# Kernel optimization log

Measured on AMD Instinct MI355X. Metric: run time of the kernel, lower is better.

The kernel has to match this reference:

```python
import jax, jax.numpy as jnp
import numpy as np

C = 5.0          # tanh clamp constant (args.c, non-trainable)
B, N, R, D = 4, 16, 64, 256  # batch, block_num, block_len, word_dim
NEG = -1e9


def setup_inputs() -> dict:
    key = jax.random.key(0)
    ks = iter(jax.random.split(key, 80))

    def W(i, o):
        # xavier-like init (torch stores (out,in); we store (in,out) and use x @ W)
        return jax.random.normal(next(ks), (i, o), jnp.float32) * np.float32(np.sqrt(2.0 / (i + o)))

    def bvec(d):
        return jax.random.normal(next(ks), (d,), jnp.float32) * 0.01

    inp = {"x": jax.random.normal(next(ks), (B, N, R, D), jnp.float32)}
    for p in ("fw", "bw"):
        inp[f"fcW_{p}"] = W(D, D);  inp[f"fcb_{p}"] = bvec(D)
        inp[f"mW1_{p}"] = W(D, D);  inp[f"mW2_{p}"] = W(D, D);  inp[f"mb_{p}"] = bvec(D)
        inp[f"s2tW1_{p}"] = W(D, D); inp[f"s2tb1_{p}"] = bvec(D)
        inp[f"s2tW_{p}"] = W(D, D);  inp[f"s2tb_{p}"] = bvec(D)
        inp[f"gW1_{p}"] = W(D, D);  inp[f"gW2_{p}"] = W(D, D);  inp[f"gb_{p}"] = bvec(D)
        inp[f"fW1_{p}"] = W(3 * D, D); inp[f"fb1_{p}"] = bvec(D)
        inp[f"fW2_{p}"] = W(3 * D, D); inp[f"fb2_{p}"] = bvec(D)
    return inp


def _mSA(x, W1, W2, b, fw):
    # x: (..., L, d) -> (..., L, d). Additive per-feature attention with strict
    # triangular mask. fw: token i attends to j > i (last row zeroed);
    # bw: token i attends to j < i (first row zeroed). Matches the torch
    # -inf mask + narrow + zero-pad construction exactly.
    L = x.shape[-2]
    xi = (x @ W1)[..., :, None, :]                 # (..., L, 1, d)
    xj = (x @ W2)[..., None, :, :]                 # (..., 1, L, d)
    f = C * jnp.tanh((xi + xj + b) / C)            # (..., i, j, d)
    i = jnp.arange(L)[:, None]
    j = jnp.arange(L)[None, :]
    allowed = (j > i) if fw else (j < i)           # (L, L)
    scores = jnp.where(allowed[..., None], f, NEG)
    att = jax.nn.softmax(scores, axis=-2)          # softmax over j
    rowvalid = (jnp.arange(L) < L - 1) if fw else (jnp.arange(L) > 0)
    att = att * rowvalid[:, None, None].astype(x.dtype)
    return jnp.einsum('...ijd,...jd->...id', att, x)


def _s2t(x, W1, b1, Wo, bo):
    # source2token self-attention: (..., L, d) -> (..., d)
    f = jax.nn.relu(x @ W1 + b1)
    a = jax.nn.softmax(f @ Wo + bo, axis=-2)
    return jnp.sum(a * x, axis=-2)


def _mblosa(x, mW1, mW2, mb, s2tW1, s2tb1, s2tW, s2tb,
            gW1, gW2, gb, fW1, fb1, fW2, fb2, fw):
    Bb, n, r, d = x.shape
    h = _mSA(x, mW1, mW2, mb, fw)                  # (B, n, r, d) intra-block
    v = _s2t(h, s2tW1, s2tb1, s2tW, s2tb)          # (B, n, d)    block summary
    o = _mSA(v, mW1, mW2, mb, fw)                  # (B, n, d)    inter-block
    G = jax.nn.sigmoid(o @ gW1 + v @ gW2 + gb)
    e = G * o + (1.0 - G) * v                      # (B, n, d)
    # torch: cat of e[i] repeated r times, then narrow(1, 0, n)
    idx = jnp.arange(n) // r
    E = e[:, idx]                                  # (B, n, d)
    # torch: flatten blocks then narrow(1, 0, n) (faithful to source)
    xf = x.reshape(Bb, n * r, d)[:, :n]
    hf = h.reshape(Bb, n * r, d)[:, :n]
    cat = jnp.concatenate([xf, hf, E], axis=-1)    # (B, n, 3d)
    fusion = jax.nn.relu(cat @ fW1 + fb1)
    Gf = jax.nn.sigmoid(cat @ fW2 + fb2)
    return Gf * fusion + (1.0 - Gf) * xf           # (B, n, d)


def reference(x,
              fcW_fw, fcb_fw, mW1_fw, mW2_fw, mb_fw, s2tW1_fw, s2tb1_fw,
              s2tW_fw, s2tb_fw, gW1_fw, gW2_fw, gb_fw, fW1_fw, fb1_fw,
              fW2_fw, fb2_fw,
              fcW_bw, fcb_bw, mW1_bw, mW2_bw, mb_bw, s2tW1_bw, s2tb1_bw,
              s2tW_bw, s2tb_bw, gW1_bw, gW2_bw, gb_bw, fW1_bw, fb1_bw,
              fW2_bw, fb2_bw):
    in_fw = jax.nn.relu(x @ fcW_fw + fcb_fw)
    in_bw = jax.nn.relu(x @ fcW_bw + fcb_bw)
    u_fw = _mblosa(in_fw, mW1_fw, mW2_fw, mb_fw, s2tW1_fw, s2tb1_fw,
                   s2tW_fw, s2tb_fw, gW1_fw, gW2_fw, gb_fw,
                   fW1_fw, fb1_fw, fW2_fw, fb2_fw, True)
    u_bw = _mblosa(in_bw, mW1_bw, mW2_bw, mb_bw, s2tW1_bw, s2tb1_bw,
                   s2tW_bw, s2tb_bw, gW1_bw, gW2_bw, gb_bw,
                   fW1_bw, fb1_bw, fW2_bw, fb2_bw, False)
    return jnp.concatenate([u_fw, u_bw], axis=-1)  # (B, n, 2d)
```

## Files before the change

kernel.cpp:

```cpp
#include <hip/hip_runtime.h>
#include <hip/hip_bf16.h>

typedef __hip_bfloat16 BF16;
typedef __attribute__((ext_vector_type(8))) short short8;
typedef __attribute__((ext_vector_type(4))) short short4v;
typedef __attribute__((ext_vector_type(4))) float f32x4;
typedef __attribute__((ext_vector_type(2))) float f32x2;

#define MFMA_B16(a,b,c) __builtin_amdgcn_mfma_f32_16x16x32_bf16((a),(b),(c),0,0,0)

#if __has_builtin(__builtin_amdgcn_exp2f)
#define EXP2F(x) __builtin_amdgcn_exp2f(x)
#else
#define EXP2F(x) __expf(0.6931471805599453f * (x))
#endif

__device__ __forceinline__ short f2bs(float f){ BF16 h = __float2bfloat16(f); return *(short*)&h; }
__device__ __forceinline__ float bs2f(short s){ BF16 h = *(BF16*)&s; return __bfloat162float(h); }

struct SrcPack { const float* s[10]; };

__global__ __launch_bounds__(256) void prep_k(SrcPack p, const float* __restrict__ xsrc,
    short* __restrict__ Oh, short* __restrict__ Ol,
    short* __restrict__ xH, short* __restrict__ xL)
{
    if (blockIdx.y < 10) {
        __shared__ float s[64][65];
        const float* W = p.s[blockIdx.y];
        short* oh = Oh + (size_t)blockIdx.y * 65536;
        short* ol = Ol + (size_t)blockIdx.y * 65536;
        int tr = (blockIdx.x >> 2) * 64, tc = (blockIdx.x & 3) * 64;
        #pragma unroll
        for (int i = 0; i < 16; i++) {
            int e = threadIdx.x + i * 256;
            int r = e >> 6, c = e & 63;
            s[c][r] = W[(size_t)(tr + r) * 256 + tc + c];
        }
        __syncthreads();
        #pragma unroll
        for (int i = 0; i < 16; i++) {
            int e = threadIdx.x + i * 256;
            int c2 = e >> 6, r2 = e & 63;
            float v = s[c2][r2];
            short hi = f2bs(v);
            short lo = f2bs(v - bs2f(hi));
            size_t oi = (size_t)(tc + c2) * 256 + tr + r2;
            oh[oi] = hi;
            ol[oi] = lo;
        }
    } else {
        size_t base0 = (size_t)(blockIdx.y - 10) * 524288
                     + (size_t)blockIdx.x * 32768 + threadIdx.x * 4;
        for (int it = 0; it < 32; it++) {
            size_t idx = base0 + (size_t)it * 1024;
            float4 f = *(const float4*)&xsrc[idx];
            float v[4] = {f.x, f.y, f.z, f.w};
            short4v h, lo;
            #pragma unroll
            for (int t = 0; t < 4; t++) {
                h[t] = f2bs(v[t]);
                lo[t] = f2bs(v[t] - bs2f(h[t]));
            }
            *(short4v*)&xH[idx] = h;
            *(short4v*)&xL[idx] = lo;
        }
    }
}

template<int AM, int OM, int RELU, int BS>
__device__ __forceinline__ void gemm_body(const void* __restrict__ A0,
    const void* __restrict__ Alo,
    const short* __restrict__ Wh, const short* __restrict__ Wl,
    const float* __restrict__ bias, void* __restrict__ O0, void* __restrict__ O1,
    int row0, int col0)
{
    constexpr int LDK = 72;
    __shared__ short sAh[64 * LDK];
    __shared__ short sAl[(AM == 0) ? 8 : 64 * LDK];
    __shared__ short sBh[64 * LDK];
    __shared__ short sBl[BS ? 8 : 64 * LDK];
    int tid = threadIdx.x;
    int w = tid >> 6, l = tid & 63;
    int m = l & 15, q = l >> 4;
    int sr = w * 16 + m;

    f32x4 acc[4];
    #pragma unroll
    for (int cf = 0; cf < 4; cf++) acc[cf] = (f32x4)(0.f);

    for (int kh = 0; kh < 4; kh++) {
        int kbase = kh * 64;
        #pragma unroll
        for (int i = 0; i < 2; i++) {
            int kl = q * 8 + 32 * i;
            size_t gofs = (size_t)(row0 + sr) * 256 + kbase + kl;
            if (AM == 1) {
                const float* src = (const float*)A0 + gofs;
                float4 f0 = *(const float4*)src;
                float4 f1 = *(const float4*)(src + 4);
                short8 vh, vl;
                float tmp[8] = {f0.x, f0.y, f0.z, f0.w, f1.x, f1.y, f1.z, f1.w};
                #pragma unroll
                for (int j = 0; j < 8; j++) {
                    vh[j] = f2bs(tmp[j]);
                    vl[j] = f2bs(tmp[j] - bs2f(vh[j]));
                }
                *(short8*)&sAh[sr * LDK + kl] = vh;
                *(short8*)&sAl[sr * LDK + kl] = vl;
            } else if (AM == 2) {
                *(short8*)&sAh[sr * LDK + kl] = *(const short8*)((const short*)A0 + gofs);
                *(short8*)&sAl[sr * LDK + kl] = *(const short8*)((const short*)Alo + gofs);
            } else {
                *(short8*)&sAh[sr * LDK + kl] = *(const short8*)((const short*)A0 + gofs);
            }
            size_t gofsB = (size_t)(col0 + sr) * 256 + kbase + kl;
            *(short8*)&sBh[sr * LDK + kl] = *(const short8*)(Wh + gofsB);
            if (!BS)
                *(short8*)&sBl[sr * LDK + kl] = *(const short8*)(Wl + gofsB);
        }
        __syncthreads();
        #pragma unroll
        for (int ch = 0; ch < 2; ch++) {
            int k = ch * 32 + q * 8;
            short8 ah = *(const short8*)&sAh[(w * 16 + m) * LDK + k];
            short8 al = (AM != 0) ? *(const short8*)&sAl[(w * 16 + m) * LDK + k] : ah;
            #pragma unroll
            for (int cf = 0; cf < 4; cf++) {
                short8 bh = *(const short8*)&sBh[(cf * 16 + m) * LDK + k];
                acc[cf] = MFMA_B16(ah, bh, acc[cf]);
                if (!BS) {
                    short8 bl = *(const short8*)&sBl[(cf * 16 + m) * LDK + k];
                    acc[cf] = MFMA_B16(ah, bl, acc[cf]);
                }
                if (AM != 0)
                    acc[cf] = MFMA_B16(al, bh, acc[cf]);
            }
        }
        __syncthreads();
    }
    #pragma unroll
    for (int cf = 0; cf < 4; cf++) {
        int col = col0 + cf * 16 + m;
        float bv = bias ? bias[col] : 0.f;
        #pragma unroll
        for (int r = 0; r < 4; r++) {
            int row = row0 + w * 16 + q * 4 + r;
            float v = acc[cf][r] + bv;
            if (RELU) v = fmaxf(v, 0.f);
            size_t oi = (size_t)row * 256 + col;
            if (OM == 0) {
                ((float*)O0)[oi] = v;
            } else if (OM == 1) {
                ((short*)O0)[oi] = f2bs(v);
            } else {
                short hi = f2bs(v);
                ((short*)O0)[oi] = hi;
                ((short*)O1)[oi] = f2bs(v - bs2f(hi));
            }
        }
    }
}

struct GDir { const void* A0; const void* Al; const short* Wh; const short* Wl;
              const float* bias; void* O0; void* O1; };

template<int AM, int OM, int RELU, int BS>
__global__ __launch_bounds__(256) void gemm_k(GDir p0, GDir p1)
{
    GDir p = blockIdx.z ? p1 : p0;
    gemm_body<AM, OM, RELU, BS>(p.A0, p.Al, p.Wh, p.Wl, p.bias, p.O0, p.O1,
                                blockIdx.x * 64, blockIdx.y * 64);
}

struct G2Dir { const float* A; const short* W1h; const short* W1l;
               const short* W2h; const short* W2l; const float* b2;
               float* C1; float* C2; };

__global__ __launch_bounds__(256) void gemm2s_k(G2Dir p0)
{
    G2Dir p = p0;
    int y = blockIdx.y;
    const short* Wh = (y < 4) ? p.W1h : p.W2h;
    const short* Wl = (y < 4) ? p.W1l : p.W2l;
    void* C = (y < 4) ? (void*)p.C1 : (void*)p.C2;
    const float* bias = (y < 4) ? nullptr : p.b2;
    gemm_body<1, 0, 0, 0>(p.A, nullptr, Wh, Wl, bias, C, nullptr, 0, (y & 3) * 64);
}

struct MbloDir { const short* Ah; const short* Al;
                 const short* W1h; const short* W2h;
                 const float* mb; short* Hh; int fw; };

__global__ __launch_bounds__(512) void mblo_k(MbloDir p0, MbloDir p1)
{
    __shared__ char smraw[33536] __attribute__((aligned(16)));
    short* gAh  = (short*)smraw;
    short* gB1h = gAh + 4608;
    short* gB2h = gAh + 9216;
    float* aP   = (float*)smraw;
    unsigned int* aQX = (unsigned int*)(smraw + 16896);

    const float KLN = -0.06931471805599453f;

    MbloDir p = blockIdx.z ? p1 : p0;
    int tid = threadIdx.x;
    int w = tid >> 6, l = tid & 63;
    int m = l & 15, q = l >> 4;
    int rh = w >> 1;
    int cb = (w & 1) * 2;
    int bn = blockIdx.x >> 1, ipar = blockIdx.x & 1;
    int row0 = bn * 64, d0 = blockIdx.y * 64;
    int srow = tid >> 3;
    int skl  = (tid & 7) * 8;

    f32x4 acc1[2], acc2[2];
    #pragma unroll
    for (int cf = 0; cf < 2; cf++) { acc1[cf] = (f32x4)(0.f); acc2[cf] = (f32x4)(0.f); }

    for (int kh = 0; kh < 4; kh++) {
        int kbase = kh * 64;
        size_t ga = (size_t)(row0 + srow) * 256 + kbase + skl;
        *(short8*)&gAh[srow * 72 + skl] = *(const short8*)(p.Ah + ga);
        size_t gb = (size_t)(d0 + srow) * 256 + kbase + skl;
        *(short8*)&gB1h[srow * 72 + skl] = *(const short8*)(p.W1h + gb);
        *(short8*)&gB2h[srow * 72 + skl] = *(const short8*)(p.W2h + gb);
        __syncthreads();
        #pragma unroll
        for (int ch = 0; ch < 2; ch++) {
            int k = ch * 32 + q * 8;
            short8 ah = *(const short8*)&gAh[(rh * 16 + m) * 72 + k];
            #pragma unroll
            for (int cf = 0; cf < 2; cf++) {
                int bofs = ((cb + cf) * 16 + m) * 72 + k;
                short8 b1 = *(const short8*)&gB1h[bofs];
                acc1[cf] = MFMA_B16(ah, b1, acc1[cf]);
                short8 b2 = *(const short8*)&gB2h[bofs];
                acc2[cf] = MFMA_B16(ah, b2, acc2[cf]);
            }
        }
        __syncthreads();
    }
    short* sQX = (short*)aQX;
    #pragma unroll
    for (int cf = 0; cf < 2; cf++) {
        int col = (cb + cf) * 16 + m;
        float mbv = p.mb[d0 + col];
        #pragma unroll
        for (int r = 0; r < 4; r++) {
            int row = rh * 16 + q * 4 + r;
            aP[row * 66 + col] = __expf(0.4f * acc1[cf][r]) * KLN;
            sQX[col * 130 + 2 * row] = f2bs(__expf(0.4f * (acc2[cf][r] + mbv)));
        }
    }
    {
        size_t gx = (size_t)(row0 + srow) * 256 + d0 + skl;
        short8 xh = *(const short8*)(p.Ah + gx);
        #pragma unroll
        for (int t = 0; t < 8; t++)
            sQX[(skl + t) * 130 + 2 * srow + 1] = xh[t];
    }
    __syncthreads();
    const unsigned int* lane_qx = &aQX[l * 65];
    #pragma unroll
    for (int t8 = 0; t8 < 4; t8++) {
        int i = ipar + 2 * (w + 8 * t8);
        float Pp = aP[i * 66 + l];
        int js = p.fw ? (i + 1) : 0;
        int je = p.fw ? 64 : i;
        float den0 = 0.f, den1 = 0.f, num0 = 0.f, num1 = 0.f;
        int j = js;
        for (; j + 4 <= je; j += 4) {
            unsigned int u0 = lane_qx[j];
            unsigned int u1 = lane_qx[j + 1];
            unsigned int u2 = lane_qx[j + 2];
            unsigned int u3 = lane_qx[j + 3];
            float q0 = bs2f((short)(u0 & 0xffff)), x0 = bs2f((short)(u0 >> 16));
            float q1 = bs2f((short)(u1 & 0xffff)), x1 = bs2f((short)(u1 >> 16));
            float q2 = bs2f((short)(u2 & 0xffff)), x2 = bs2f((short)(u2 >> 16));
            float q3 = bs2f((short)(u3 & 0xffff)), x3 = bs2f((short)(u3 >> 16));
            float w0 = EXP2F(__builtin_amdgcn_rcpf(fmaf(Pp, q0, KLN)));
            float w1 = EXP2F(__builtin_amdgcn_rcpf(fmaf(Pp, q1, KLN)));
            float w2 = EXP2F(__builtin_amdgcn_rcpf(fmaf(Pp, q2, KLN)));
            float w3 = EXP2F(__builtin_amdgcn_rcpf(fmaf(Pp, q3, KLN)));
            den0 += w0; num0 = fmaf(w0, x0, num0);
            den1 += w1; num1 = fmaf(w1, x1, num1);
            den0 += w2; num0 = fmaf(w2, x2, num0);
            den1 += w3; num1 = fmaf(w3, x3, num1);
        }
        for (; j < je; j++) {
            unsigned int u0 = lane_qx[j];
            float q0 = bs2f((short)(u0 & 0xffff)), x0 = bs2f((short)(u0 >> 16));
            float wgt = EXP2F(__builtin_amdgcn_rcpf(fmaf(Pp, q0, KLN)));
            den0 += wgt; num0 = fmaf(wgt, x0, num0);
        }
        float den = den0 + den1, num = num0 + num1;
        bool valid = p.fw ? (i < 63) : (i > 0);
        float out = valid ? (num * __builtin_amdgcn_rcpf(den)) : 0.f;
        p.Hh[(size_t)(row0 + i) * 256 + d0 + l] = f2bs(out);
    }
}

struct PoolDir { const short* T1; const short* Wh; const float* bias;
                 const short* Hh; float* V; };

__global__ __launch_bounds__(256) void s2t_pool_k(PoolDir p0, PoolDir p1)
{
    __shared__ char smraw[37888] __attribute__((aligned(16)));
    short* gAh = (short*)smraw;
    short* gBh = gAh + 4608;
    float* aL = (float*)smraw;
    float* aH = aL + 4352;
    float* rm = aL + 8704;
    float* rd = aL + 8960;
    float* rn = aL + 9216;

    PoolDir p = blockIdx.z ? p1 : p0;
    int tid = threadIdx.x;
    int w = tid >> 6, l = tid & 63;
    int m = l & 15, q = l >> 4;
    int sr = w * 16 + m;
    int row0 = blockIdx.x * 64, d0 = blockIdx.y * 64;

    f32x4 acc[4];
    #pragma unroll
    for (int cf = 0; cf < 4; cf++) acc[cf] = (f32x4)(0.f);

    for (int kh = 0; kh < 4; kh++) {
        int kbase = kh * 64;
        #pragma unroll
        for (int i = 0; i < 2; i++) {
            int kl = q * 8 + 32 * i;
            *(short8*)&gAh[sr * 72 + kl] =
                *(const short8*)(p.T1 + (size_t)(row0 + sr) * 256 + kbase + kl);
            *(short8*)&gBh[sr * 72 + kl] =
                *(const short8*)(p.Wh + (size_t)(d0 + sr) * 256 + kbase + kl);
        }
        __syncthreads();
        #pragma unroll
        for (int ch = 0; ch < 2; ch++) {
            int k = ch * 32 + q * 8;
            short8 ah = *(const short8*)&gAh[(w * 16 + m) * 72 + k];
            #pragma unroll
            for (int cf = 0; cf < 4; cf++) {
                short8 bh = *(const short8*)&gBh[(cf * 16 + m) * 72 + k];
                acc[cf] = MFMA_B16(ah, bh, acc[cf]);
            }
        }
        __syncthreads();
    }
    #pragma unroll
    for (int cf = 0; cf < 4; cf++) {
        int col = cf * 16 + m;
        float bv = p.bias[d0 + col];
        #pragma unroll
        for (int r = 0; r < 4; r++) {
            int row = w * 16 + q * 4 + r;
            aL[row * 68 + col] = acc[cf][r] + bv;
        }
    }
    #pragma unroll
    for (int it = 0; it < 2; it++) {
        int e = tid + it * 256;
        int j = e >> 3, d8 = (e & 7) * 8;
        short8 xh = *(const short8*)(p.Hh + (size_t)(row0 + j) * 256 + d0 + d8);
        #pragma unroll
        for (int t = 0; t < 8; t++)
            aH[j * 68 + d8 + t] = bs2f(xh[t]);
    }
    __syncthreads();
    int dl = tid & 63, rq = tid >> 6;
    float mx = -1e30f, den = 0.f, num = 0.f;
    #pragma unroll
    for (int rr = 0; rr < 16; rr++) {
        int r = rq * 16 + rr;
        float lv = aL[r * 68 + dl];
        float hv = aH[r * 68 + dl];
        if (lv > mx) {
            float sc = __expf(mx - lv);
            den *= sc; num *= sc; mx = lv;
        }
        float wgt = __expf(lv - mx);
        den += wgt; num += wgt * hv;
    }
    rm[rq * 64 + dl] = mx; rd[rq * 64 + dl] = den; rn[rq * 64 + dl] = num;
    __syncthreads();
    if (rq == 0) {
        float M = fmaxf(fmaxf(rm[dl], rm[64 + dl]), fmaxf(rm[128 + dl], rm[192 + dl]));
        float D = 0.f, Nn = 0.f;
        #pragma unroll
        for (int k = 0; k < 4; k++) {
            float sc = __expf(rm[k * 64 + dl] - M);
            D += rd[k * 64 + dl] * sc;
            Nn += rn[k * 64 + dl] * sc;
        }
        p.V[(size_t)blockIdx.x * 256 + d0 + dl] = Nn / D;
    }
}

struct GateDir { const float* vW1; const float* vW2; const float* V;
                 const float* gW1; const float* gW2; const float* gb;
                 float* E0; int fw; };

__global__ __launch_bounds__(256) void attn2gate_k(GateDir p0, GateDir p1)
{
    GateDir p = blockIdx.z ? p1 : p0;
    __shared__ float so[256], sv[256], red[4][64];
    int b = blockIdx.x, k = threadIdx.x;
    float o = 0.f;
    if (p.fw) {
        float qv = p.vW1[(size_t)(b * 16) * 256 + k];
        float den = 0.f, num = 0.f;
        for (int j = 1; j < 16; j++) {
            float z = (qv + p.vW2[(size_t)(b * 16 + j) * 256 + k]) * 0.2f;
            float e2 = __expf(2.f * z);
            float t = 1.f - 2.f / (e2 + 1.f);
            float wgt = __expf(5.f * t);
            den += wgt; num += wgt * p.V[(size_t)(b * 16 + j) * 256 + k];
        }
        o = num / den;
    }
    so[k] = o;
    sv[k] = p.V[(size_t)(b * 16) * 256 + k];
    __syncthreads();
    int c = k & 63, ks = k >> 6;
    int gc = blockIdx.y * 64 + c;
    float acc = 0.f;
    int k0 = ks * 64;
    #pragma unroll 8
    for (int kk = 0; kk < 64; kk++) {
        int kx = k0 + kk;
        acc += so[kx] * p.gW1[(size_t)kx * 256 + gc] + sv[kx] * p.gW2[(size_t)kx * 256 + gc];
    }
    red[ks][c] = acc;
    __syncthreads();
    if (ks == 0) {
        float a = red[0][c] + red[1][c] + red[2][c] + red[3][c] + p.gb[gc];
        float G = 1.f / (1.f + __expf(-a));
        p.E0[b * 256 + gc] = G * so[gc] + (1.f - G) * sv[gc];
    }
}

struct FuseDir { const short* INh; const short* INl; const short* Hh;
                 const float* E0; const float* fW1; const float* fb1;
                 const float* fW2; const float* fb2; };

__global__ __launch_bounds__(256) void fusion_k(FuseDir p0, FuseDir p1, float* __restrict__ out)
{
    FuseDir p = blockIdx.z ? p1 : p0;
    __shared__ float cat[768];
    __shared__ float red1[4][64], red2[4][64];
    int bt = blockIdx.x, b = bt >> 4, t = bt & 15;
    int c = threadIdx.x & 63, ks = threadIdx.x >> 6;
    int gc = blockIdx.y * 64 + c;
    size_t xrow = ((size_t)b * 1024 + t) * 256;
    cat[threadIdx.x]       = bs2f(p.INh[xrow + threadIdx.x]) + bs2f(p.INl[xrow + threadIdx.x]);
    cat[256 + threadIdx.x] = bs2f(p.Hh[xrow + threadIdx.x]);
    cat[512 + threadIdx.x] = p.E0[b * 256 + threadIdx.x];
    __syncthreads();
    float a1 = 0.f, a2 = 0.f;
    int k0 = ks * 192;
    #pragma unroll 8
    for (int kk = 0; kk < 192; kk++) {
        int k = k0 + kk;
        float cv = cat[k];
        a1 += cv * p.fW1[(size_t)k * 256 + gc];
        a2 += cv * p.fW2[(size_t)k * 256 + gc];
    }
    red1[ks][c] = a1; red2[ks][c] = a2;
    __syncthreads();
    if (ks == 0) {
        float s1 = red1[0][c] + red1[1][c] + red1[2][c] + red1[3][c] + p.fb1[gc];
        float s2 = red2[0][c] + red2[1][c] + red2[2][c] + red2[3][c] + p.fb2[gc];
        float fus = fmaxf(s1, 0.f);
        float Gf = 1.f / (1.f + __expf(-s2));
        float u = Gf * fus + (1.f - Gf) * cat[gc];
        out[((size_t)(b * 16 + t)) * 512 + (size_t)blockIdx.z * 256 + gc] = u;
    }
}

extern "C" void kernel_launch(void* const* d_in, const int* in_sizes, int n_in,
                              void* d_out, int out_size, void* d_ws, size_t ws_size,
                              hipStream_t stream)
{
    const float* x = (const float*)d_in[0];
    char* base = (char*)d_ws;
    auto alloc = [&](size_t bytes){ void* r = base; base += (bytes + 255) & ~255ULL; return r; };
    short* inH = (short*)alloc(2 * 1048576 * 2);
    short* inL = (short*)alloc(2 * 1048576 * 2);
    short* hH  = (short*)alloc(2 * 1048576 * 2);
    short* t1  = (short*)alloc(2 * 1048576 * 2);
    short* xH  = (short*)alloc(1048576 * 2);
    short* xL  = (short*)alloc(1048576 * 2);
    short* wtH = (short*)alloc(10 * 65536 * 2);
    short* wtL = (short*)alloc(10 * 65536 * 2);
    float* v   = (float*)alloc(2 * 16384 * 4);
    float* vW1 = (float*)alloc(2 * 16384 * 4);
    float* vW2 = (float*)alloc(2 * 16384 * 4);
    float* E0  = (float*)alloc(2 * 1024 * 4);

    SrcPack sp;
    const int src_idx[5] = {0, 2, 3, 5, 7};
    for (int p = 0; p < 2; p++)
        for (int i = 0; i < 5; i++)
            sp.s[p * 5 + i] = (const float*)d_in[1 + p * 16 + src_idx[i]];
    prep_k<<<dim3(16, 12), 256, 0, stream>>>(sp, x, wtH, wtL, xH, xL);

    GDir fc[2], s2t1[2];
    MbloDir mbd[2];
    PoolDir pld[2];
    G2Dir g2d[2];
    GateDir gtd[2];
    FuseDir fsd[2];
    for (int p = 0; p < 2; p++) {
        int bi = 1 + p * 16;
        const float* fcb   = (const float*)d_in[bi + 1];
        const float* mb    = (const float*)d_in[bi + 4];
        const float* s2tb1 = (const float*)d_in[bi + 6];
        const float* s2tb  = (const float*)d_in[bi + 8];
        size_t po = (size_t)p * 1048576;
        const short* W0h = wtH + (size_t)(p * 5 + 0) * 65536, *W0l = wtL + (size_t)(p * 5 + 0) * 65536;
        const short* W1h = wtH + (size_t)(p * 5 + 1) * 65536, *W1l = wtL + (size_t)(p * 5 + 1) * 65536;
        const short* W2h = wtH + (size_t)(p * 5 + 2) * 65536, *W2l = wtL + (size_t)(p * 5 + 2) * 65536;
        const short* W3h = wtH + (size_t)(p * 5 + 3) * 65536;
        const short* W4h = wtH + (size_t)(p * 5 + 4) * 65536;

        fc[p]   = { xH, xL, W0h, W0l, fcb, inH + po, inL + po };
        mbd[p]  = { inH + po, inL + po, W1h, W2h, mb, hH + po, (p == 0) };
        s2t1[p] = { hH + po, nullptr, W3h, nullptr, s2tb1, t1 + po, nullptr };
        pld[p]  = { t1 + po, W4h, s2tb, hH + po, v + p * 16384 };
        g2d[p]  = { v + p * 16384, W1h, W1l, W2h, W2l, mb, vW1 + p * 16384, vW2 + p * 16384 };
        gtd[p]  = { vW1 + p * 16384, vW2 + p * 16384, v + p * 16384,
                    (const float*)d_in[bi + 9], (const float*)d_in[bi + 10],
                    (const float*)d_in[bi + 11], E0 + p * 1024, (p == 0) };
        fsd[p]  = { inH + po, inL + po, hH + po, E0 + p * 1024,
                    (const float*)d_in[bi + 12], (const float*)d_in[bi + 13],
                    (const float*)d_in[bi + 14], (const float*)d_in[bi + 15] };
    }

    gemm_k<2, 2, 1, 0><<<dim3(64, 4, 2), 256, 0, stream>>>(fc[0], fc[1]);
    mblo_k<<<dim3(128, 4, 2), 512, 0, stream>>>(mbd[0], mbd[1]);
    gemm_k<0, 1, 1, 1><<<dim3(64, 4, 2), 256, 0, stream>>>(s2t1[0], s2t1[1]);
    s2t_pool_k<<<dim3(64, 4, 2), 256, 0, stream>>>(pld[0], pld[1]);
    gemm2s_k<<<dim3(1, 8, 1), 256, 0, stream>>>(g2d[0]);
    attn2gate_k<<<dim3(4, 4, 2), 256, 0, stream>>>(gtd[0], gtd[1]);
    fusion_k<<<dim3(64, 4, 2), 256, 0, stream>>>(fsd[0], fsd[1], (float*)d_out);
}
```

Before: 207.5 us.

## Drop split-bf16 x precomputation and low-part activation buffers

Stops pre-converting x into hi/lo bf16 halves in prep_k and has the fc GEMM read the fp32 input directly (AM=1), writing only the bf16 high part of the activation. The low-part activation buffer is removed, so mblo and fusion read only the high part. The gemm2s workspace is also shrunk to a single direction. This cuts memory traffic and one prep phase, but fc outputs lose their lo correction, which lowers precision in mblo and fusion.

```diff
diff --git a/kernel.cpp b/kernel.cpp
--- a/kernel.cpp
+++ b/kernel.cpp
@@ -3,9 +3,7 @@
 
 typedef __hip_bfloat16 BF16;
 typedef __attribute__((ext_vector_type(8))) short short8;
-typedef __attribute__((ext_vector_type(4))) short short4v;
 typedef __attribute__((ext_vector_type(4))) float f32x4;
-typedef __attribute__((ext_vector_type(2))) float f32x2;
 
 #define MFMA_B16(a,b,c) __builtin_amdgcn_mfma_f32_16x16x32_bf16((a),(b),(c),0,0,0)
 
@@ -20,50 +18,31 @@
 
 struct SrcPack { const float* s[10]; };
 
-__global__ __launch_bounds__(256) void prep_k(SrcPack p, const float* __restrict__ xsrc,
-    short* __restrict__ Oh, short* __restrict__ Ol,
-    short* __restrict__ xH, short* __restrict__ xL)
-{
-    if (blockIdx.y < 10) {
-        __shared__ float s[64][65];
-        const float* W = p.s[blockIdx.y];
-        short* oh = Oh + (size_t)blockIdx.y * 65536;
-        short* ol = Ol + (size_t)blockIdx.y * 65536;
-        int tr = (blockIdx.x >> 2) * 64, tc = (blockIdx.x & 3) * 64;
-        #pragma unroll
-        for (int i = 0; i < 16; i++) {
-            int e = threadIdx.x + i * 256;
-            int r = e >> 6, c = e & 63;
-            s[c][r] = W[(size_t)(tr + r) * 256 + tc + c];
-        }
-        __syncthreads();
-        #pragma unroll
-        for (int i = 0; i < 16; i++) {
-            int e = threadIdx.x + i * 256;
-            int c2 = e >> 6, r2 = e & 63;
-            float v = s[c2][r2];
-            short hi = f2bs(v);
-            short lo = f2bs(v - bs2f(hi));
-            size_t oi = (size_t)(tc + c2) * 256 + tr + r2;
-            oh[oi] = hi;
-            ol[oi] = lo;
-        }
-    } else {
-        size_t base0 = (size_t)(blockIdx.y - 10) * 524288
-                     + (size_t)blockIdx.x * 32768 + threadIdx.x * 4;
-        for (int it = 0; it < 32; it++) {
-            size_t idx = base0 + (size_t)it * 1024;
-            float4 f = *(const float4*)&xsrc[idx];
-            float v[4] = {f.x, f.y, f.z, f.w};
-            short4v h, lo;
-            #pragma unroll
-            for (int t = 0; t < 4; t++) {
-                h[t] = f2bs(v[t]);
-                lo[t] = f2bs(v[t] - bs2f(h[t]));
-            }
-            *(short4v*)&xH[idx] = h;
-            *(short4v*)&xL[idx] = lo;
-        }
+__global__ __launch_bounds__(256) void prep_k(SrcPack p, short* __restrict__ Oh,
+                                              short* __restrict__ Ol)
+{
+    __shared__ float s[64][65];
+    const float* W = p.s[blockIdx.y];
+    short* oh = Oh + (size_t)blockIdx.y * 65536;
+    short* ol = Ol + (size_t)blockIdx.y * 65536;
+    int tr = (blockIdx.x >> 2) * 64, tc = (blockIdx.x & 3) * 64;
+    #pragma unroll
+    for (int i = 0; i < 16; i++) {
+        int e = threadIdx.x + i * 256;
+        int r = e >> 6, c = e & 63;
+        s[c][r] = W[(size_t)(tr + r) * 256 + tc + c];
+    }
+    __syncthreads();
+    #pragma unroll
+    for (int i = 0; i < 16; i++) {
+        int e = threadIdx.x + i * 256;
+        int c2 = e >> 6, r2 = e & 63;
+        float v = s[c2][r2];
+        short hi = f2bs(v);
+        short lo = f2bs(v - bs2f(hi));
+        size_t oi = (size_t)(tc + c2) * 256 + tr + r2;
+        oh[oi] = hi;
+        ol[oi] = lo;
     }
 }
 
@@ -187,7 +166,7 @@
     gemm_body<1, 0, 0, 0>(p.A, nullptr, Wh, Wl, bias, C, nullptr, 0, (y & 3) * 64);
 }
 
-struct MbloDir { const short* Ah; const short* Al;
+struct MbloDir { const short* Ah;
                  const short* W1h; const short* W2h;
                  const float* mb; short* Hh; int fw; };
 
@@ -440,7 +419,7 @@
     }
 }
 
-struct FuseDir { const short* INh; const short* INl; const short* Hh;
+struct FuseDir { const short* INh; const short* Hh;
                  const float* E0; const float* fW1; const float* fb1;
                  const float* fW2; const float* fb2; };
 
@@ -453,7 +432,7 @@
     int c = threadIdx.x & 63, ks = threadIdx.x >> 6;
     int gc = blockIdx.y * 64 + c;
     size_t xrow = ((size_t)b * 1024 + t) * 256;
-    cat[threadIdx.x]       = bs2f(p.INh[xrow + threadIdx.x]) + bs2f(p.INl[xrow + threadIdx.x]);
+    cat[threadIdx.x]       = bs2f(p.INh[xrow + threadIdx.x]);
     cat[256 + threadIdx.x] = bs2f(p.Hh[xrow + threadIdx.x]);
     cat[512 + threadIdx.x] = p.E0[b * 256 + threadIdx.x];
     __syncthreads();
@@ -486,16 +465,13 @@
     char* base = (char*)d_ws;
     auto alloc = [&](size_t bytes){ void* r = base; base += (bytes + 255) & ~255ULL; return r; };
     short* inH = (short*)alloc(2 * 1048576 * 2);
-    short* inL = (short*)alloc(2 * 1048576 * 2);
     short* hH  = (short*)alloc(2 * 1048576 * 2);
     short* t1  = (short*)alloc(2 * 1048576 * 2);
-    short* xH  = (short*)alloc(1048576 * 2);
-    short* xL  = (short*)alloc(1048576 * 2);
     short* wtH = (short*)alloc(10 * 65536 * 2);
     short* wtL = (short*)alloc(10 * 65536 * 2);
     float* v   = (float*)alloc(2 * 16384 * 4);
-    float* vW1 = (float*)alloc(2 * 16384 * 4);
-    float* vW2 = (float*)alloc(2 * 16384 * 4);
+    float* vW1 = (float*)alloc(16384 * 4);
+    float* vW2 = (float*)alloc(16384 * 4);
     float* E0  = (float*)alloc(2 * 1024 * 4);
 
     SrcPack sp;
@@ -503,12 +479,12 @@
     for (int p = 0; p < 2; p++)
         for (int i = 0; i < 5; i++)
             sp.s[p * 5 + i] = (const float*)d_in[1 + p * 16 + src_idx[i]];
-    prep_k<<<dim3(16, 12), 256, 0, stream>>>(sp, x, wtH, wtL, xH, xL);
+    prep_k<<<dim3(16, 10), 256, 0, stream>>>(sp, wtH, wtL);
 
     GDir fc[2], s2t1[2];
     MbloDir mbd[2];
     PoolDir pld[2];
-    G2Dir g2d[2];
+    G2Dir g2d;
     GateDir gtd[2];
     FuseDir fsd[2];
     for (int p = 0; p < 2; p++) {
@@ -524,24 +500,24 @@
         const short* W3h = wtH + (size_t)(p * 5 + 3) * 65536;
         const short* W4h = wtH + (size_t)(p * 5 + 4) * 65536;
 
-        fc[p]   = { xH, xL, W0h, W0l, fcb, inH + po, inL + po };
-        mbd[p]  = { inH + po, inL + po, W1h, W2h, mb, hH + po, (p == 0) };
+        fc[p]   = { x, nullptr, W0h, W0l, fcb, inH + po, nullptr };
+        mbd[p]  = { inH + po, W1h, W2h, mb, hH + po, (p == 0) };
         s2t1[p] = { hH + po, nullptr, W3h, nullptr, s2tb1, t1 + po, nullptr };
         pld[p]  = { t1 + po, W4h, s2tb, hH + po, v + p * 16384 };
-        g2d[p]  = { v + p * 16384, W1h, W1l, W2h, W2l, mb, vW1 + p * 16384, vW2 + p * 16384 };
-        gtd[p]  = { vW1 + p * 16384, vW2 + p * 16384, v + p * 16384,
+        if (p == 0) g2d = { v, W1h, W1l, W2h, W2l, mb, vW1, vW2 };
+        gtd[p]  = { vW1, vW2, v + p * 16384,
                     (const float*)d_in[bi + 9], (const float*)d_in[bi + 10],
                     (const float*)d_in[bi + 11], E0 + p * 1024, (p == 0) };
-        fsd[p]  = { inH + po, inL + po, hH + po, E0 + p * 1024,
+        fsd[p]  = { inH + po, hH + po, E0 + p * 1024,
                     (const float*)d_in[bi + 12], (const float*)d_in[bi + 13],
                     (const float*)d_in[bi + 14], (const float*)d_in[bi + 15] };
     }
 
-    gemm_k<2, 2, 1, 0><<<dim3(64, 4, 2), 256, 0, stream>>>(fc[0], fc[1]);
+    gemm_k<1, 1, 1, 0><<<dim3(64, 4, 2), 256, 0, stream>>>(fc[0], fc[1]);
     mblo_k<<<dim3(128, 4, 2), 512, 0, stream>>>(mbd[0], mbd[1]);
     gemm_k<0, 1, 1, 1><<<dim3(64, 4, 2), 256, 0, stream>>>(s2t1[0], s2t1[1]);
     s2t_pool_k<<<dim3(64, 4, 2), 256, 0, stream>>>(pld[0], pld[1]);
-    gemm2s_k<<<dim3(1, 8, 1), 256, 0, stream>>>(g2d[0]);
+    gemm2s_k<<<dim3(1, 8, 1), 256, 0, stream>>>(g2d);
     attn2gate_k<<<dim3(4, 4, 2), 256, 0, stream>>>(gtd[0], gtd[1]);
     fusion_k<<<dim3(64, 4, 2), 256, 0, stream>>>(fsd[0], fsd[1], (float*)d_out);
 }
```

New measurement: 206.1 us. No clear change (-0.7%).
